# Performance work log

Measured on AMD Instinct MI355X. Metric: run time of the kernel, lower is better.

The kernel has to match this reference:

```python
import jax, jax.numpy as jnp
import numpy as np
import math

B, S, D, H, NH = 2, 2048, 1024, 16, 8
DK = D // H


def setup_inputs() -> dict:
    key = jax.random.key(0)
    ks = jax.random.split(key, 10)
    s = 1.0 / math.sqrt(D)
    return {
        "x": jax.random.normal(ks[0], (B, S, D), jnp.float32),
        "Wq": jax.random.normal(ks[1], (D, D), jnp.float32) * s,
        "bq": jnp.zeros((D,), jnp.float32),
        "Wk": jax.random.normal(ks[2], (D, D), jnp.float32) * s,
        "bk": jnp.zeros((D,), jnp.float32),
        "Wv": jax.random.normal(ks[3], (D, D), jnp.float32) * s,
        "bv": jnp.zeros((D,), jnp.float32),
        "Wo": jax.random.normal(ks[4], (D, D), jnp.float32) * s,
        "bo": jnp.zeros((D,), jnp.float32),
        "R": jax.random.normal(ks[5], (NH, DK), jnp.float32),
    }


def reference(x, Wq, bq, Wk, bk, Wv, bv, Wo, bo, R):
    b, s, _ = x.shape
    # projections -> [B, S, H, DK]
    Q = (x @ Wq + bq).reshape(b, s, H, DK)
    K = (x @ Wk + bk).reshape(b, s, H, DK)
    V = (x @ Wv + bv).reshape(b, s, H, DK)
    # LSH buckets: argmax over random projections -> [B, S, H] -> [B, H, S]
    qb = jnp.argmax(jnp.einsum('bshd,nd->bshn', Q, R), axis=-1).transpose(0, 2, 1)
    kb = jnp.argmax(jnp.einsum('bshd,nd->bshn', K, R), axis=-1).transpose(0, 2, 1)
    # bucket-equality mask [B, H, S, S]
    mask = qb[:, :, :, None] == kb[:, :, None, :]
    # attention: [B, H, S, S]
    scores = jnp.einsum('bihd,bjhd->bhij', Q, K) / jnp.sqrt(jnp.float32(DK))
    scores = jnp.where(mask, scores, -jnp.inf)
    probs = jax.nn.softmax(scores, axis=-1)
    out = jnp.einsum('bhij,bjhd->bihd', probs, V).reshape(b, s, D)
    return out @ Wo + bo
```

## Files before the change

kernel.cpp:

```cpp
#include <hip/hip_runtime.h>
#include <hip/hip_bf16.h>


typedef __bf16 bf16;
typedef __bf16 bf16x8 __attribute__((ext_vector_type(8)));
typedef __bf16 bf16x4 __attribute__((ext_vector_type(4)));
typedef float f32x4 __attribute__((ext_vector_type(4)));

#define DEV static __device__ __forceinline__

DEV f32x4 zero4() { f32x4 z; z[0]=0.f; z[1]=0.f; z[2]=0.f; z[3]=0.f; return z; }

DEV f32x4 mfma_bf16(bf16x8 a, bf16x8 b, f32x4 c) {
  return __builtin_amdgcn_mfma_f32_16x16x32_bf16(a, b, c, 0, 0, 0);
}

DEV void load_lds16(const bf16* g, bf16* l) {
  __builtin_amdgcn_global_load_lds(
      (const __attribute__((address_space(1))) void*)g,
      (__attribute__((address_space(3))) void*)l, 16, 0, 0);
}

#define B_  2
#define S_  2048
#define D_  1024
#define H_  16
#define NH_ 8
#define DK_ 64
#define M_  4096
#define QPAD 2560
#define NQT  40

__global__ void k_cast_split(const float* __restrict__ x, bf16* __restrict__ xh,
                             bf16* __restrict__ xm, bf16* __restrict__ xl) {
  int i = (blockIdx.x * 256 + threadIdx.x) * 4;
  f32x4 v = *(const f32x4*)(x + i);
  bf16x4 oh, om, ol;
#pragma unroll
  for (int j = 0; j < 4; j++) {
    float f = v[j];
    bf16 h = (bf16)f;
    float rm = f - (float)h;
    bf16 m = (bf16)rm;
    float rl = rm - (float)m;
    oh[j] = h; om[j] = m; ol[j] = (bf16)rl;
  }
  *(bf16x4*)(xh + i) = oh;
  *(bf16x4*)(xm + i) = om;
  *(bf16x4*)(xl + i) = ol;
}

__global__ void k_transW(const float* __restrict__ W0, const float* __restrict__ W1,
                         const float* __restrict__ W2, const float* __restrict__ W3,
                         bf16* __restrict__ T0, bf16* __restrict__ T1,
                         bf16* __restrict__ T2, bf16* __restrict__ T3) {
  __shared__ float tile[64][65];
  const float* W = blockIdx.z == 0 ? W0 : blockIdx.z == 1 ? W1 : blockIdx.z == 2 ? W2 : W3;
  bf16* Wt = blockIdx.z == 0 ? T0 : blockIdx.z == 1 ? T1 : blockIdx.z == 2 ? T2 : T3;
  int k0 = blockIdx.x * 64, n0 = blockIdx.y * 64;
  int c = threadIdx.x & 63, r4 = threadIdx.x >> 6;
#pragma unroll
  for (int i = 0; i < 16; i++) {
    int r = r4 * 16 + i;
    tile[r][c] = W[(k0 + r) * D_ + n0 + c];
  }
  __syncthreads();
#pragma unroll
  for (int i = 0; i < 16; i++) {
    int r = r4 * 16 + i;
    Wt[(n0 + r) * D_ + k0 + c] = (bf16)tile[c][r];
  }
}

__global__ void k_computeP(const float* __restrict__ Wq, const float* __restrict__ Wk,
                           const float* __restrict__ R, float* __restrict__ P) {
  int d = blockIdx.x;
  int t = threadIdx.x;
  int hn = t & 127, h = hn >> 3, n = hn & 7;
  const float* W = (t < 128) ? Wq : Wk;
  const float* wrow = W + d * D_ + h * 64;
  const float* rrow = R + n * 64;
  float acc = 0.f;
#pragma unroll 8
  for (int k = 0; k < 64; k++) acc += wrow[k] * rrow[k];
  P[d * 256 + t] = acc;
}

__global__ void k_transP(const float* __restrict__ P, bf16* __restrict__ Pth,
                         bf16* __restrict__ Ptm, bf16* __restrict__ Ptl) {
  __shared__ float tile[64][65];
  int k0 = blockIdx.x * 64, n0 = blockIdx.y * 64;
  int c = threadIdx.x & 63, r4 = threadIdx.x >> 6;
#pragma unroll
  for (int i = 0; i < 16; i++) {
    int r = r4 * 16 + i;
    tile[r][c] = P[(k0 + r) * 256 + n0 + c];
  }
  __syncthreads();
#pragma unroll
  for (int i = 0; i < 16; i++) {
    int r = r4 * 16 + i;
    float v = tile[c][r];
    bf16 h = (bf16)v;
    float rm = v - (float)h;
    bf16 m = (bf16)rm;
    bf16 l = (bf16)(rm - (float)m);
    int o = (n0 + r) * D_ + k0 + c;
    Pth[o] = h; Ptm[o] = m; Ptl[o] = l;
  }
}

__global__ void k_bterm(const float* __restrict__ bq, const float* __restrict__ bk,
                        const float* __restrict__ R, float* __restrict__ bt) {
  int t = threadIdx.x;
  const float* b = (t < 128) ? bq : bk;
  int hn = t & 127, h = hn >> 3, n = hn & 7;
  float acc = 0.f;
#pragma unroll 8
  for (int k = 0; k < 64; k++) acc += b[h * 64 + k] * R[n * 64 + k];
  bt[t] = acc;
}

__global__ __launch_bounds__(256) void k_lgemm(const bf16* __restrict__ xh,
                                               const bf16* __restrict__ xm,
                                               const bf16* __restrict__ xl,
                                               const bf16* __restrict__ Pth,
                                               const bf16* __restrict__ Ptm,
                                               const bf16* __restrict__ Ptl,
                                               const float* __restrict__ bt,
                                               int* __restrict__ qb,
                                               int* __restrict__ kb) {
  __shared__ bf16 Ls[6][64 * 32];
  const int t = threadIdx.x;
  const int m0 = blockIdx.x * 64, n0 = blockIdx.y * 64;
  const int lane = t & 63, w = t >> 6;
  const int lm = lane & 15, qd = lane >> 4;
  const bf16* src6[6] = {xh, xm, xl, Pth, Ptm, Ptl};
  const int srow = lane >> 2, sseg = lane & 3;

  f32x4 acc[4];
#pragma unroll
  for (int nb = 0; nb < 4; nb++) acc[nb] = zero4();

  for (int k0 = 0; k0 < D_; k0 += 32) {
    __syncthreads();
#pragma unroll
    for (int r3 = 0; r3 < 6; r3++) {
      int ii = r3 * 4 + w;
      int tt = ii >> 2, qq = ii & 3;
      int base = (tt < 3 ? m0 : n0) + qq * 16 + srow;
      load_lds16(&src6[tt][base * D_ + k0 + sseg * 8], &Ls[tt][qq * 16 * 32]);
    }
    __syncthreads();
    bf16x8 af[3], bfr[3][4];
#pragma unroll
    for (int i3 = 0; i3 < 3; i3++) {
      af[i3] = *(const bf16x8*)&Ls[i3][(w * 16 + lm) * 32 + qd * 8];
#pragma unroll
      for (int nb = 0; nb < 4; nb++)
        bfr[i3][nb] = *(const bf16x8*)&Ls[3 + i3][(nb * 16 + lm) * 32 + qd * 8];
    }
#pragma unroll
    for (int nb = 0; nb < 4; nb++) {
      f32x4 a = acc[nb];
      a = mfma_bf16(af[0], bfr[0][nb], a);
      a = mfma_bf16(af[0], bfr[1][nb], a);
      a = mfma_bf16(af[1], bfr[0][nb], a);
      a = mfma_bf16(af[0], bfr[2][nb], a);
      a = mfma_bf16(af[2], bfr[0][nb], a);
      a = mfma_bf16(af[1], bfr[1][nb], a);
      acc[nb] = a;
    }
  }

#pragma unroll
  for (int nb = 0; nb < 4; nb++) {
    int n = n0 + nb * 16 + lm;
    float btv = bt[n];
#pragma unroll
    for (int r = 0; r < 4; r++) {
      float v = acc[nb][r] + btv;
      int idx = lm & 7;
#pragma unroll
      for (int mask = 1; mask <= 4; mask <<= 1) {
        float pv = __shfl_xor(v, mask);
        int pi = __shfl_xor(idx, mask);
        if (pv > v || (pv == v && pi < idx)) { v = pv; idx = pi; }
      }
      if ((lm & 7) == 0) {
        int m = m0 + w * 16 + qd * 4 + r;
        int g = n >> 3;
        int sel = g >> 4, head = g & 15;
        int bb = m >> 11, s = m & 2047;
        (sel ? kb : qb)[(bb * H_ + head) * S_ + s] = idx;
      }
    }
  }
}

__global__ __launch_bounds__(256) void k_sort(const int* __restrict__ qb,
                                              const int* __restrict__ kb,
                                              int* __restrict__ qidx,
                                              int* __restrict__ kidx,
                                              int2* __restrict__ meta) {
  __shared__ int cnt[8][257];
  __shared__ int bst[2][9];
  __shared__ int tot[2][8];
  const int bh = blockIdx.x;
  const int t = threadIdx.x;
  for (int which = 0; which < 2; which++) {
    const int* src = (which ? kb : qb) + bh * S_;
    int* dst = (which ? kidx : qidx) + bh * QPAD;
    for (int i = t; i < QPAD; i += 256) dst[i] = -1;
    int vals[8];
    int lc[8] = {0, 0, 0, 0, 0, 0, 0, 0};
#pragma unroll
    for (int j = 0; j < 8; j++) { int b = src[t * 8 + j]; vals[j] = b; lc[b]++; }
#pragma unroll
    for (int b = 0; b < 8; b++) cnt[b][t] = lc[b];
    __syncthreads();
    if (t < 8) {
      int run = 0;
      for (int i = 0; i < 256; i++) { int c = cnt[t][i]; cnt[t][i] = run; run += c; }
      tot[which][t] = run;
    }
    __syncthreads();
    if (t == 0) {
      int pos = 0;
      for (int b = 0; b < 8; b++) {
        bst[which][b] = pos;
        pos += (tot[which][b] + 63) & ~63;
      }
      bst[which][8] = pos;
    }
    __syncthreads();
    int run2[8] = {0, 0, 0, 0, 0, 0, 0, 0};
#pragma unroll
    for (int j = 0; j < 8; j++) {
      int b = vals[j];
      int pos = bst[which][b] + cnt[b][t] + run2[b]++;
      dst[pos] = t * 8 + j;
    }
    __syncthreads();
  }
  if (t == 0) {
    for (int tt = 0; tt < NQT; tt++) meta[bh * NQT + tt] = make_int2(0, 0);
    for (int b = 0; b < 8; b++) {
      int t0 = bst[0][b] >> 6;
      int nt = ((tot[0][b] + 63) & ~63) >> 6;
      int ks = bst[1][b];
      int nkt = (tot[1][b] + 63) >> 6;
      for (int tt = t0; tt < t0 + nt; tt++)
        meta[bh * NQT + tt] = make_int2(ks, nkt);
    }
  }
}

template <int MODE>
__global__ __launch_bounds__(256) void k_gemm128(
    const bf16* __restrict__ A,
    const bf16* __restrict__ Bt0, const bf16* __restrict__ Bt1,
    const bf16* __restrict__ Bt2,
    const float* __restrict__ bi0, const float* __restrict__ bi1,
    const float* __restrict__ bi2,
    void* __restrict__ o0, void* __restrict__ o1, void* __restrict__ o2) {
  __shared__ bf16 Al[128 * 32];
  __shared__ bf16 Bl[128 * 32];
  const int t = threadIdx.x;
  const int lane = t & 63, w = t >> 6;
  const int m0 = blockIdx.x * 128;
  const int mat = blockIdx.y >> 3;
  const int n0 = (blockIdx.y & 7) * 128;
  const bf16* Bt = mat == 0 ? Bt0 : (mat == 1 ? Bt1 : Bt2);
  const float* bias = mat == 0 ? bi0 : (mat == 1 ? bi1 : bi2);
  void* out = mat == 0 ? o0 : (mat == 1 ? o1 : o2);
  const int lm = lane & 15, qd = lane >> 4;
  const int wm = w >> 1, wn = w & 1;
  const int srow = lane >> 2, sseg = lane & 3;

  f32x4 acc[4][4];
#pragma unroll
  for (int i = 0; i < 4; i++)
#pragma unroll
    for (int j = 0; j < 4; j++) acc[i][j] = zero4();

  for (int k0 = 0; k0 < D_; k0 += 32) {
    __syncthreads();
    load_lds16(&A[(m0 + w * 16 + srow) * D_ + k0 + sseg * 8],
               &Al[(w * 16) * 32]);
    load_lds16(&A[(m0 + 64 + w * 16 + srow) * D_ + k0 + sseg * 8],
               &Al[(64 + w * 16) * 32]);
    load_lds16(&Bt[(n0 + w * 16 + srow) * D_ + k0 + sseg * 8],
               &Bl[(w * 16) * 32]);
    load_lds16(&Bt[(n0 + 64 + w * 16 + srow) * D_ + k0 + sseg * 8],
               &Bl[(64 + w * 16) * 32]);
    __syncthreads();
    bf16x8 af[4], bfr[4];
#pragma unroll
    for (int i = 0; i < 4; i++)
      af[i] = *(const bf16x8*)&Al[(wm * 64 + i * 16 + lm) * 32 + qd * 8];
#pragma unroll
    for (int j = 0; j < 4; j++)
      bfr[j] = *(const bf16x8*)&Bl[(wn * 64 + j * 16 + lm) * 32 + qd * 8];
#pragma unroll
    for (int i = 0; i < 4; i++)
#pragma unroll
      for (int j = 0; j < 4; j++) acc[i][j] = mfma_bf16(af[i], bfr[j], acc[i][j]);
  }

#pragma unroll
  for (int j = 0; j < 4; j++) {
    int n = n0 + wn * 64 + j * 16 + lm;
    float bv = bias[n];
#pragma unroll
    for (int i = 0; i < 4; i++) {
      int mbase = m0 + wm * 64 + i * 16 + qd * 4;
#pragma unroll
      for (int r = 0; r < 4; r++) {
        int m = mbase + r;
        float v = acc[i][j][r] + bv;
        if (MODE == 0) {
          int bb = m >> 11, s = m & 2047, hh = n >> 6, d = n & 63;
          ((bf16*)out)[((bb * H_ + hh) * S_ + s) * DK_ + d] = (bf16)v;
        } else {
          ((float*)out)[m * D_ + n] = v;
        }
      }
    }
  }
}

__global__ __launch_bounds__(256) void k_attn(const bf16* __restrict__ Q,
                                              const bf16* __restrict__ K,
                                              const bf16* __restrict__ V,
                                              const int* __restrict__ qidx,
                                              const int* __restrict__ kidx,
                                              const int2* __restrict__ meta,
                                              bf16* __restrict__ O) {
  constexpr int LDK = 72;
  __shared__ bf16 Kl[64 * LDK];
  __shared__ bf16 Vl[64 * LDK];
  __shared__ bf16 Pl[64 * LDK];
  __shared__ int kbl[64];
  __shared__ int qsl[64];
  const int t = threadIdx.x;
  const int qt = blockIdx.x, h = blockIdx.y, b = blockIdx.z;
  const int lane = t & 63, w = t >> 6;
  const int lm = lane & 15, qd = lane >> 4;
  const int bh = b * H_ + h;

  const int2 mt = meta[bh * NQT + qt];
  const int kstart = mt.x, nkt = mt.y;

  if (t < 64) qsl[t] = qidx[bh * QPAD + qt * 64 + t];
  __syncthreads();

  if (nkt == 0) {
#pragma unroll
    for (int r = 0; r < 4; r++) {
      int qs = qsl[w * 16 + qd * 4 + r];
      if (qs >= 0)
#pragma unroll
        for (int nb = 0; nb < 4; nb++)
          O[((b * S_ + qs) * H_ + h) * DK_ + nb * 16 + lm] = (bf16)0.f;
    }
    return;
  }

  int qrow = qsl[w * 16 + lm];
  const bf16* Qp = Q + (bh * S_ + (qrow < 0 ? 0 : qrow)) * DK_;
  bf16x8 qf0 = *(const bf16x8*)(Qp + qd * 8);
  bf16x8 qf1 = *(const bf16x8*)(Qp + 32 + qd * 8);

  f32x4 oacc[4];
  float mrun[4], lrun[4];
#pragma unroll
  for (int nb = 0; nb < 4; nb++) oacc[nb] = zero4();
#pragma unroll
  for (int r = 0; r < 4; r++) { mrun[r] = -1e30f; lrun[r] = 0.f; }

  const bf16* Kbase = K + bh * S_ * DK_;
  const bf16* Vbase = V + bh * S_ * DK_;
  const int* kix = kidx + bh * QPAD + kstart;

  for (int kt = 0; kt < nkt; kt++) {
    const int kt0 = kt * 64;
    __syncthreads();
    if (t < 64) kbl[t] = kix[kt0 + t];
#pragma unroll
    for (int ss = 0; ss < 2; ss++) {
      int seg = t + ss * 256;
      int row = seg >> 3, sg = seg & 7;
      int ki = kix[kt0 + row]; ki = ki < 0 ? 0 : ki;
      *(bf16x8*)&Kl[row * LDK + sg * 8] =
          *(const bf16x8*)&Kbase[ki * DK_ + sg * 8];
    }
#pragma unroll
    for (int ss = 0; ss < 2; ss++) {
      int seg = t + ss * 256;
      int vrow = seg & 63, vsg = seg >> 6;
      int ki = kix[kt0 + vrow]; ki = ki < 0 ? 0 : ki;
      bf16x8 v8 = *(const bf16x8*)&Vbase[ki * DK_ + vsg * 8];
#pragma unroll
      for (int j = 0; j < 8; j++) Vl[(vsg * 8 + j) * LDK + vrow] = v8[j];
    }
    __syncthreads();

    f32x4 sc[4];
#pragma unroll
    for (int nb = 0; nb < 4; nb++) {
      bf16x8 kf0 = *(const bf16x8*)&Kl[(nb * 16 + lm) * LDK + qd * 8];
      bf16x8 kf1 = *(const bf16x8*)&Kl[(nb * 16 + lm) * LDK + 32 + qd * 8];
      f32x4 z = zero4();
      z = mfma_bf16(qf0, kf0, z);
      z = mfma_bf16(qf1, kf1, z);
      sc[nb] = z;
    }
#pragma unroll
    for (int nb = 0; nb < 4; nb++) {
      bool valid = kbl[nb * 16 + lm] >= 0;
#pragma unroll
      for (int r = 0; r < 4; r++)
        sc[nb][r] = valid ? sc[nb][r] * 0.125f : -1e30f;
    }
    float mnew[4], alpha[4], rs[4];
#pragma unroll
    for (int r = 0; r < 4; r++) {
      float tm = fmaxf(fmaxf(sc[0][r], sc[1][r]), fmaxf(sc[2][r], sc[3][r]));
      tm = fmaxf(tm, __shfl_xor(tm, 1));
      tm = fmaxf(tm, __shfl_xor(tm, 2));
      tm = fmaxf(tm, __shfl_xor(tm, 4));
      tm = fmaxf(tm, __shfl_xor(tm, 8));
      mnew[r] = fmaxf(mrun[r], tm);
      alpha[r] = __expf(mrun[r] - mnew[r]);
      mrun[r] = mnew[r];
      rs[r] = 0.f;
    }
#pragma unroll
    for (int nb = 0; nb < 4; nb++)
#pragma unroll
      for (int r = 0; r < 4; r++) {
        float p = (sc[nb][r] > -1e29f) ? __expf(sc[nb][r] - mnew[r]) : 0.f;
        sc[nb][r] = p;
        rs[r] += p;
      }
#pragma unroll
    for (int r = 0; r < 4; r++) {
      float s = rs[r];
      s += __shfl_xor(s, 1);
      s += __shfl_xor(s, 2);
      s += __shfl_xor(s, 4);
      s += __shfl_xor(s, 8);
      lrun[r] = lrun[r] * alpha[r] + s;
    }
#pragma unroll
    for (int nb = 0; nb < 4; nb++)
#pragma unroll
      for (int r = 0; r < 4; r++) oacc[nb][r] *= alpha[r];
#pragma unroll
    for (int nb = 0; nb < 4; nb++)
#pragma unroll
      for (int r = 0; r < 4; r++)
        Pl[(w * 16 + qd * 4 + r) * LDK + nb * 16 + lm] = (bf16)sc[nb][r];
    __syncthreads();
    bf16x8 pa0 = *(const bf16x8*)&Pl[(w * 16 + lm) * LDK + qd * 8];
    bf16x8 pa1 = *(const bf16x8*)&Pl[(w * 16 + lm) * LDK + 32 + qd * 8];
#pragma unroll
    for (int nb = 0; nb < 4; nb++) {
      bf16x8 vf0 = *(const bf16x8*)&Vl[(nb * 16 + lm) * LDK + qd * 8];
      bf16x8 vf1 = *(const bf16x8*)&Vl[(nb * 16 + lm) * LDK + 32 + qd * 8];
      oacc[nb] = mfma_bf16(pa0, vf0, oacc[nb]);
      oacc[nb] = mfma_bf16(pa1, vf1, oacc[nb]);
    }
  }
#pragma unroll
  for (int r = 0; r < 4; r++) {
    int qs = qsl[w * 16 + qd * 4 + r];
    if (qs < 0) continue;
    float l = lrun[r];
    float inv = (l > 0.f) ? 1.f / l : 0.f;
#pragma unroll
    for (int nb = 0; nb < 4; nb++)
      O[((b * S_ + qs) * H_ + h) * DK_ + nb * 16 + lm] = (bf16)(oacc[nb][r] * inv);
  }
}

extern "C" void kernel_launch(void* const* d_in, const int* in_sizes, int n_in,
                              void* d_out, int out_size, void* d_ws, size_t ws_size,
                              hipStream_t stream) {
  (void)in_sizes; (void)n_in; (void)out_size; (void)ws_size;
  const float* x  = (const float*)d_in[0];
  const float* Wq = (const float*)d_in[1];
  const float* bq = (const float*)d_in[2];
  const float* Wk = (const float*)d_in[3];
  const float* bk = (const float*)d_in[4];
  const float* Wv = (const float*)d_in[5];
  const float* bv = (const float*)d_in[6];
  const float* Wo = (const float*)d_in[7];
  const float* bo = (const float*)d_in[8];
  const float* R  = (const float*)d_in[9];

  char* ws = (char*)d_ws;
  bf16*  xh   = (bf16*)(ws + 0);
  bf16*  Qb   = (bf16*)(ws + 8388608);
  bf16*  Kb   = (bf16*)(ws + 16777216);
  bf16*  Vb   = (bf16*)(ws + 25165824);
  bf16*  Ob   = (bf16*)(ws + 33554432);
  bf16*  xm   = (bf16*)(ws + 33554432);
  bf16*  Wtq  = (bf16*)(ws + 41943040);
  bf16*  Wtk  = (bf16*)(ws + 44040192);
  bf16*  Wtv  = (bf16*)(ws + 46137344);
  bf16*  Wto  = (bf16*)(ws + 48234496);
  float* Pfull= (float*)(ws + 50331648);
  int*   qbuf = (int*)(ws + 51380224);
  int*   kbuf = (int*)(ws + 51642368);
  float* bt   = (float*)(ws + 51904512);
  bf16*  Pth  = (bf16*)(ws + 51905536);
  bf16*  Ptm  = (bf16*)(ws + 52429824);
  bf16*  Ptl  = (bf16*)(ws + 52954112);
  int*   qidxp= (int*)(ws + 53478400);
  int*   kidxp= (int*)(ws + 53806080);
  int2*  meta = (int2*)(ws + 54133760);
  bf16*  xl   = (bf16*)d_out;

  k_cast_split<<<dim3(4096), dim3(256), 0, stream>>>(x, xh, xm, xl);
  k_transW<<<dim3(16, 16, 4), dim3(256), 0, stream>>>(Wq, Wk, Wv, Wo,
                                                      Wtq, Wtk, Wtv, Wto);
  k_computeP<<<dim3(1024), dim3(256), 0, stream>>>(Wq, Wk, R, Pfull);
  k_bterm<<<dim3(1), dim3(256), 0, stream>>>(bq, bk, R, bt);
  k_transP<<<dim3(16, 4), dim3(256), 0, stream>>>(Pfull, Pth, Ptm, Ptl);

  k_lgemm<<<dim3(64, 4), dim3(256), 0, stream>>>(xh, xm, xl, Pth, Ptm, Ptl,
                                                 bt, qbuf, kbuf);
  k_sort<<<dim3(32), dim3(256), 0, stream>>>(qbuf, kbuf, qidxp, kidxp, meta);

  k_gemm128<0><<<dim3(32, 24), dim3(256), 0, stream>>>(
      xh, Wtq, Wtk, Wtv, bq, bk, bv, (void*)Qb, (void*)Kb, (void*)Vb);

  k_attn<<<dim3(NQT, H_, B_), dim3(256), 0, stream>>>(Qb, Kb, Vb, qidxp, kidxp,
                                                      meta, Ob);

  k_gemm128<2><<<dim3(32, 8), dim3(256), 0, stream>>>(
      Ob, Wto, Wto, Wto, bo, bo, bo, d_out, d_out, d_out);
}
```

Before: 251.5 us.

## Fuse prep kernels, merge LSH and QKV GEMMs, parallelize sort scan, smaller out-proj tiles

Combines the weight transpose, x cast, the projection matrix P and the bias term into a single prep launch. P is now computed directly in transposed, split form, so the fp32 intermediate and its transpose pass are gone. The LSH bucket GEMM now splits x into hi/mid/lo inside the kernel and shares one grid with the QKV projection GEMM, which removes the xm/xl buffers and a launch. The sort's serial per-bucket prefix scan becomes a wave-level shuffle scan, and the output projection uses 64x128 tiles to get more blocks. Risks are load imbalance between the two block types in the merged kernel and the LDS footprint of the larger shared arrays.

```diff
diff --git a/kernel.cpp b/kernel.cpp
--- a/kernel.cpp
+++ b/kernel.cpp
@@ -19,6 +19,13 @@
   __builtin_amdgcn_global_load_lds(
       (const __attribute__((address_space(1))) void*)g,
       (__attribute__((address_space(3))) void*)l, 16, 0, 0);
+}
+
+DEV void split3(float f, bf16& h, bf16& m, bf16& l) {
+  h = (bf16)f;
+  float rm = f - (float)h;
+  m = (bf16)rm;
+  l = (bf16)(rm - (float)m);
 }
 
 #define B_  2
@@ -31,168 +38,234 @@
 #define QPAD 2560
 #define NQT  40
 
-__global__ void k_cast_split(const float* __restrict__ x, bf16* __restrict__ xh,
-                             bf16* __restrict__ xm, bf16* __restrict__ xl) {
-  int i = (blockIdx.x * 256 + threadIdx.x) * 4;
-  f32x4 v = *(const f32x4*)(x + i);
-  bf16x4 oh, om, ol;
-#pragma unroll
-  for (int j = 0; j < 4; j++) {
-    float f = v[j];
-    bf16 h = (bf16)f;
-    float rm = f - (float)h;
-    bf16 m = (bf16)rm;
-    float rl = rm - (float)m;
-    oh[j] = h; om[j] = m; ol[j] = (bf16)rl;
-  }
-  *(bf16x4*)(xh + i) = oh;
-  *(bf16x4*)(xm + i) = om;
-  *(bf16x4*)(xl + i) = ol;
-}
-
-__global__ void k_transW(const float* __restrict__ W0, const float* __restrict__ W1,
-                         const float* __restrict__ W2, const float* __restrict__ W3,
-                         bf16* __restrict__ T0, bf16* __restrict__ T1,
-                         bf16* __restrict__ T2, bf16* __restrict__ T3) {
+__global__ __launch_bounds__(256) void k_prep(
+    const float* __restrict__ Wq, const float* __restrict__ Wk,
+    const float* __restrict__ Wv, const float* __restrict__ Wo,
+    const float* __restrict__ x, const float* __restrict__ bq,
+    const float* __restrict__ bk, const float* __restrict__ R,
+    bf16* __restrict__ Wtq, bf16* __restrict__ Wtk,
+    bf16* __restrict__ Wtv, bf16* __restrict__ Wto,
+    bf16* __restrict__ xh, bf16* __restrict__ Pth, bf16* __restrict__ Ptm,
+    bf16* __restrict__ Ptl, float* __restrict__ bt) {
   __shared__ float tile[64][65];
-  const float* W = blockIdx.z == 0 ? W0 : blockIdx.z == 1 ? W1 : blockIdx.z == 2 ? W2 : W3;
-  bf16* Wt = blockIdx.z == 0 ? T0 : blockIdx.z == 1 ? T1 : blockIdx.z == 2 ? T2 : T3;
-  int k0 = blockIdx.x * 64, n0 = blockIdx.y * 64;
-  int c = threadIdx.x & 63, r4 = threadIdx.x >> 6;
-#pragma unroll
-  for (int i = 0; i < 16; i++) {
-    int r = r4 * 16 + i;
-    tile[r][c] = W[(k0 + r) * D_ + n0 + c];
-  }
-  __syncthreads();
-#pragma unroll
-  for (int i = 0; i < 16; i++) {
-    int r = r4 * 16 + i;
-    Wt[(n0 + r) * D_ + k0 + c] = (bf16)tile[c][r];
-  }
-}
-
-__global__ void k_computeP(const float* __restrict__ Wq, const float* __restrict__ Wk,
-                           const float* __restrict__ R, float* __restrict__ P) {
-  int d = blockIdx.x;
-  int t = threadIdx.x;
-  int hn = t & 127, h = hn >> 3, n = hn & 7;
-  const float* W = (t < 128) ? Wq : Wk;
-  const float* wrow = W + d * D_ + h * 64;
-  const float* rrow = R + n * 64;
-  float acc = 0.f;
+  __shared__ float Rl[512];
+  const int t = threadIdx.x;
+  const int z = blockIdx.z;
+  if (z < 4) {
+    const float* W = z == 0 ? Wq : z == 1 ? Wk : z == 2 ? Wv : Wo;
+    bf16* Wt = z == 0 ? Wtq : z == 1 ? Wtk : z == 2 ? Wtv : Wto;
+    int k0 = blockIdx.x * 64, n0 = blockIdx.y * 64;
+    int c = t & 63, r4 = t >> 6;
+#pragma unroll
+    for (int i = 0; i < 16; i++) {
+      int r = r4 * 16 + i;
+      tile[r][c] = W[(k0 + r) * D_ + n0 + c];
+    }
+    __syncthreads();
+#pragma unroll
+    for (int i = 0; i < 16; i++) {
+      int r = r4 * 16 + i;
+      Wt[(n0 + r) * D_ + k0 + c] = (bf16)tile[c][r];
+    }
+  } else if (z == 4) {
+    int bid = blockIdx.y * 16 + blockIdx.x;
+    int base = bid * 16384 + t * 4;
+#pragma unroll 4
+    for (int it = 0; it < 16; it++) {
+      int i = base + it * 1024;
+      f32x4 v = *(const f32x4*)(x + i);
+      bf16x4 o;
+#pragma unroll
+      for (int j = 0; j < 4; j++) o[j] = (bf16)v[j];
+      *(bf16x4*)(xh + i) = o;
+    }
+  } else {
+    int bid = blockIdx.y * 16 + blockIdx.x;
+    if (bid >= 64) return;
+    Rl[t] = R[t];
+    Rl[t + 256] = R[t + 256];
+    __syncthreads();
+    const int d0 = bid * 16;
+    const int sel = t >> 7, hn = t & 127, h = hn >> 3, n = hn & 7;
+    const float* W = sel ? Wk : Wq;
+    const float* Rr = &Rl[n * 64];
+    bf16x8 vh[2], vm[2], vl[2];
+#pragma unroll
+    for (int dl = 0; dl < 16; dl++) {
+      const float* wr = W + (d0 + dl) * D_ + h * 64;
+      float acc = 0.f;
+#pragma unroll
+      for (int k = 0; k < 64; k += 4) {
+        f32x4 wv = *(const f32x4*)(wr + k);
+        acc += (wv[0] * Rr[k] + wv[1] * Rr[k + 1]) +
+               (wv[2] * Rr[k + 2] + wv[3] * Rr[k + 3]);
+      }
+      bf16 hh, mm, ll;
+      split3(acc, hh, mm, ll);
+      vh[dl >> 3][dl & 7] = hh;
+      vm[dl >> 3][dl & 7] = mm;
+      vl[dl >> 3][dl & 7] = ll;
+    }
+    *(bf16x8*)&Pth[t * D_ + d0] = vh[0];
+    *(bf16x8*)&Pth[t * D_ + d0 + 8] = vh[1];
+    *(bf16x8*)&Ptm[t * D_ + d0] = vm[0];
+    *(bf16x8*)&Ptm[t * D_ + d0 + 8] = vm[1];
+    *(bf16x8*)&Ptl[t * D_ + d0] = vl[0];
+    *(bf16x8*)&Ptl[t * D_ + d0 + 8] = vl[1];
+    if (bid == 0) {
+      const float* bb = sel ? bk : bq;
+      float acc = 0.f;
 #pragma unroll 8
-  for (int k = 0; k < 64; k++) acc += wrow[k] * rrow[k];
-  P[d * 256 + t] = acc;
-}
-
-__global__ void k_transP(const float* __restrict__ P, bf16* __restrict__ Pth,
-                         bf16* __restrict__ Ptm, bf16* __restrict__ Ptl) {
-  __shared__ float tile[64][65];
-  int k0 = blockIdx.x * 64, n0 = blockIdx.y * 64;
-  int c = threadIdx.x & 63, r4 = threadIdx.x >> 6;
-#pragma unroll
-  for (int i = 0; i < 16; i++) {
-    int r = r4 * 16 + i;
-    tile[r][c] = P[(k0 + r) * 256 + n0 + c];
-  }
-  __syncthreads();
-#pragma unroll
-  for (int i = 0; i < 16; i++) {
-    int r = r4 * 16 + i;
-    float v = tile[c][r];
-    bf16 h = (bf16)v;
-    float rm = v - (float)h;
-    bf16 m = (bf16)rm;
-    bf16 l = (bf16)(rm - (float)m);
-    int o = (n0 + r) * D_ + k0 + c;
-    Pth[o] = h; Ptm[o] = m; Ptl[o] = l;
-  }
-}
-
-__global__ void k_bterm(const float* __restrict__ bq, const float* __restrict__ bk,
-                        const float* __restrict__ R, float* __restrict__ bt) {
-  int t = threadIdx.x;
-  const float* b = (t < 128) ? bq : bk;
-  int hn = t & 127, h = hn >> 3, n = hn & 7;
-  float acc = 0.f;
-#pragma unroll 8
-  for (int k = 0; k < 64; k++) acc += b[h * 64 + k] * R[n * 64 + k];
-  bt[t] = acc;
-}
-
-__global__ __launch_bounds__(256) void k_lgemm(const bf16* __restrict__ xh,
-                                               const bf16* __restrict__ xm,
-                                               const bf16* __restrict__ xl,
-                                               const bf16* __restrict__ Pth,
-                                               const bf16* __restrict__ Ptm,
-                                               const bf16* __restrict__ Ptl,
-                                               const float* __restrict__ bt,
-                                               int* __restrict__ qb,
-                                               int* __restrict__ kb) {
-  __shared__ bf16 Ls[6][64 * 32];
+      for (int k = 0; k < 64; k++) acc += bb[h * 64 + k] * Rr[k];
+      bt[t] = acc;
+    }
+  }
+}
+
+__global__ __launch_bounds__(256) void k_main(
+    const float* __restrict__ x, const bf16* __restrict__ xh,
+    const bf16* __restrict__ Wtq, const bf16* __restrict__ Wtk,
+    const bf16* __restrict__ Wtv, const float* __restrict__ bq,
+    const float* __restrict__ bk, const float* __restrict__ bv,
+    const bf16* __restrict__ Pth, const bf16* __restrict__ Ptm,
+    const bf16* __restrict__ Ptl, const float* __restrict__ bt,
+    bf16* __restrict__ Qb, bf16* __restrict__ Kb, bf16* __restrict__ Vb,
+    int* __restrict__ qb, int* __restrict__ kb) {
+  __shared__ __align__(16) bf16 SA[3][2048];
+  __shared__ __align__(16) bf16 SB[3][2048];
   const int t = threadIdx.x;
-  const int m0 = blockIdx.x * 64, n0 = blockIdx.y * 64;
   const int lane = t & 63, w = t >> 6;
   const int lm = lane & 15, qd = lane >> 4;
-  const bf16* src6[6] = {xh, xm, xl, Pth, Ptm, Ptl};
   const int srow = lane >> 2, sseg = lane & 3;
 
-  f32x4 acc[4];
-#pragma unroll
-  for (int nb = 0; nb < 4; nb++) acc[nb] = zero4();
-
-  for (int k0 = 0; k0 < D_; k0 += 32) {
-    __syncthreads();
-#pragma unroll
-    for (int r3 = 0; r3 < 6; r3++) {
-      int ii = r3 * 4 + w;
-      int tt = ii >> 2, qq = ii & 3;
-      int base = (tt < 3 ? m0 : n0) + qq * 16 + srow;
-      load_lds16(&src6[tt][base * D_ + k0 + sseg * 8], &Ls[tt][qq * 16 * 32]);
-    }
-    __syncthreads();
-    bf16x8 af[3], bfr[3][4];
-#pragma unroll
-    for (int i3 = 0; i3 < 3; i3++) {
-      af[i3] = *(const bf16x8*)&Ls[i3][(w * 16 + lm) * 32 + qd * 8];
-#pragma unroll
-      for (int nb = 0; nb < 4; nb++)
-        bfr[i3][nb] = *(const bf16x8*)&Ls[3 + i3][(nb * 16 + lm) * 32 + qd * 8];
+  if (blockIdx.y < 24) {
+    if (blockIdx.x >= 32) return;
+    bf16* Al = &SA[0][0];
+    bf16* Bl = &SB[0][0];
+    const int m0 = blockIdx.x * 128;
+    const int mat = blockIdx.y >> 3;
+    const int n0 = (blockIdx.y & 7) * 128;
+    const bf16* Bt = mat == 0 ? Wtq : (mat == 1 ? Wtk : Wtv);
+    const float* bias = mat == 0 ? bq : (mat == 1 ? bk : bv);
+    bf16* out = mat == 0 ? Qb : (mat == 1 ? Kb : Vb);
+    const int wm = w >> 1, wn = w & 1;
+
+    f32x4 acc[4][4];
+#pragma unroll
+    for (int i = 0; i < 4; i++)
+#pragma unroll
+      for (int j = 0; j < 4; j++) acc[i][j] = zero4();
+
+    for (int k0 = 0; k0 < D_; k0 += 32) {
+      __syncthreads();
+      load_lds16(&xh[(m0 + w * 16 + srow) * D_ + k0 + sseg * 8],
+                 &Al[(w * 16) * 32]);
+      load_lds16(&xh[(m0 + 64 + w * 16 + srow) * D_ + k0 + sseg * 8],
+                 &Al[(64 + w * 16) * 32]);
+      load_lds16(&Bt[(n0 + w * 16 + srow) * D_ + k0 + sseg * 8],
+                 &Bl[(w * 16) * 32]);
+      load_lds16(&Bt[(n0 + 64 + w * 16 + srow) * D_ + k0 + sseg * 8],
+                 &Bl[(64 + w * 16) * 32]);
+      __syncthreads();
+      bf16x8 af[4], bfr[4];
+#pragma unroll
+      for (int i = 0; i < 4; i++)
+        af[i] = *(const bf16x8*)&Al[(wm * 64 + i * 16 + lm) * 32 + qd * 8];
+#pragma unroll
+      for (int j = 0; j < 4; j++)
+        bfr[j] = *(const bf16x8*)&Bl[(wn * 64 + j * 16 + lm) * 32 + qd * 8];
+#pragma unroll
+      for (int i = 0; i < 4; i++)
+#pragma unroll
+        for (int j = 0; j < 4; j++)
+          acc[i][j] = mfma_bf16(af[i], bfr[j], acc[i][j]);
+    }
+#pragma unroll
+    for (int j = 0; j < 4; j++) {
+      int n = n0 + wn * 64 + j * 16 + lm;
+      float bv2 = bias[n];
+#pragma unroll
+      for (int i = 0; i < 4; i++) {
+        int mbase = m0 + wm * 64 + i * 16 + qd * 4;
+#pragma unroll
+        for (int r = 0; r < 4; r++) {
+          int m = mbase + r;
+          int bb = m >> 11, s = m & 2047, hh = n >> 6, d = n & 63;
+          out[((bb * H_ + hh) * S_ + s) * DK_ + d] = (bf16)(acc[i][j][r] + bv2);
+        }
+      }
+    }
+  } else {
+    const int m0 = blockIdx.x * 64, n0 = (blockIdx.y - 24) * 64;
+    f32x4 acc[4];
+#pragma unroll
+    for (int nb = 0; nb < 4; nb++) acc[nb] = zero4();
+    const int xrow = t >> 2, xc8 = (t & 3) * 8;
+
+    for (int k0 = 0; k0 < D_; k0 += 32) {
+      __syncthreads();
+      f32x4 xa = *(const f32x4*)&x[(m0 + xrow) * D_ + k0 + xc8];
+      f32x4 xb2 = *(const f32x4*)&x[(m0 + xrow) * D_ + k0 + xc8 + 4];
+      bf16x8 vh, vm, vl;
+#pragma unroll
+      for (int j = 0; j < 4; j++) {
+        bf16 hh, mm, ll;
+        split3(xa[j], hh, mm, ll);
+        vh[j] = hh; vm[j] = mm; vl[j] = ll;
+        split3(xb2[j], hh, mm, ll);
+        vh[4 + j] = hh; vm[4 + j] = mm; vl[4 + j] = ll;
+      }
+      *(bf16x8*)&SA[0][xrow * 32 + xc8] = vh;
+      *(bf16x8*)&SA[1][xrow * 32 + xc8] = vm;
+      *(bf16x8*)&SA[2][xrow * 32 + xc8] = vl;
+      load_lds16(&Pth[(n0 + w * 16 + srow) * D_ + k0 + sseg * 8],
+                 &SB[0][(w * 16) * 32]);
+      load_lds16(&Ptm[(n0 + w * 16 + srow) * D_ + k0 + sseg * 8],
+                 &SB[1][(w * 16) * 32]);
+      load_lds16(&Ptl[(n0 + w * 16 + srow) * D_ + k0 + sseg * 8],
+                 &SB[2][(w * 16) * 32]);
+      __syncthreads();
+      bf16x8 af[3], bfr[3][4];
+#pragma unroll
+      for (int i3 = 0; i3 < 3; i3++) {
+        af[i3] = *(const bf16x8*)&SA[i3][(w * 16 + lm) * 32 + qd * 8];
+#pragma unroll
+        for (int nb = 0; nb < 4; nb++)
+          bfr[i3][nb] = *(const bf16x8*)&SB[i3][(nb * 16 + lm) * 32 + qd * 8];
+      }
+#pragma unroll
+      for (int nb = 0; nb < 4; nb++) {
+        f32x4 a = acc[nb];
+        a = mfma_bf16(af[0], bfr[0][nb], a);
+        a = mfma_bf16(af[0], bfr[1][nb], a);
+        a = mfma_bf16(af[1], bfr[0][nb], a);
+        a = mfma_bf16(af[0], bfr[2][nb], a);
+        a = mfma_bf16(af[2], bfr[0][nb], a);
+        a = mfma_bf16(af[1], bfr[1][nb], a);
+        acc[nb] = a;
+      }
     }
 #pragma unroll
     for (int nb = 0; nb < 4; nb++) {
-      f32x4 a = acc[nb];
-      a = mfma_bf16(af[0], bfr[0][nb], a);
-      a = mfma_bf16(af[0], bfr[1][nb], a);
-      a = mfma_bf16(af[1], bfr[0][nb], a);
-      a = mfma_bf16(af[0], bfr[2][nb], a);
-      a = mfma_bf16(af[2], bfr[0][nb], a);
-      a = mfma_bf16(af[1], bfr[1][nb], a);
-      acc[nb] = a;
-    }
-  }
-
-#pragma unroll
-  for (int nb = 0; nb < 4; nb++) {
-    int n = n0 + nb * 16 + lm;
-    float btv = bt[n];
-#pragma unroll
-    for (int r = 0; r < 4; r++) {
-      float v = acc[nb][r] + btv;
-      int idx = lm & 7;
-#pragma unroll
-      for (int mask = 1; mask <= 4; mask <<= 1) {
-        float pv = __shfl_xor(v, mask);
-        int pi = __shfl_xor(idx, mask);
-        if (pv > v || (pv == v && pi < idx)) { v = pv; idx = pi; }
-      }
-      if ((lm & 7) == 0) {
-        int m = m0 + w * 16 + qd * 4 + r;
-        int g = n >> 3;
-        int sel = g >> 4, head = g & 15;
-        int bb = m >> 11, s = m & 2047;
-        (sel ? kb : qb)[(bb * H_ + head) * S_ + s] = idx;
+      int n = n0 + nb * 16 + lm;
+      float btv = bt[n];
+#pragma unroll
+      for (int r = 0; r < 4; r++) {
+        float v = acc[nb][r] + btv;
+        int idx = lm & 7;
+#pragma unroll
+        for (int mask = 1; mask <= 4; mask <<= 1) {
+          float pv = __shfl_xor(v, mask);
+          int pi = __shfl_xor(idx, mask);
+          if (pv > v || (pv == v && pi < idx)) { v = pv; idx = pi; }
+        }
+        if ((lm & 7) == 0) {
+          int m = m0 + w * 16 + qd * 4 + r;
+          int g = n >> 3;
+          int sel = g >> 4, head = g & 15;
+          int bb = m >> 11, s = m & 2047;
+          (sel ? kb : qb)[(bb * H_ + head) * S_ + s] = idx;
+        }
       }
     }
   }
@@ -208,6 +281,7 @@
   __shared__ int tot[2][8];
   const int bh = blockIdx.x;
   const int t = threadIdx.x;
+  const int lane = t & 63, w = t >> 6;
   for (int which = 0; which < 2; which++) {
     const int* src = (which ? kb : qb) + bh * S_;
     int* dst = (which ? kidx : qidx) + bh * QPAD;
@@ -219,10 +293,20 @@
 #pragma unroll
     for (int b = 0; b < 8; b++) cnt[b][t] = lc[b];
     __syncthreads();
-    if (t < 8) {
-      int run = 0;
-      for (int i = 0; i < 256; i++) { int c = cnt[t][i]; cnt[t][i] = run; run += c; }
-      tot[which][t] = run;
+    for (int bb = w; bb < 8; bb += 4) {
+      int carry = 0;
+      for (int round = 0; round < 4; round++) {
+        int v = cnt[bb][round * 64 + lane];
+        int inc = v;
+#pragma unroll
+        for (int off = 1; off < 64; off <<= 1) {
+          int u = __shfl_up(inc, off);
+          if (lane >= off) inc += u;
+        }
+        cnt[bb][round * 64 + lane] = carry + inc - v;
+        carry += __shfl(inc, 63);
+      }
+      if (lane == 0) tot[which][bb] = carry;
     }
     __syncthreads();
     if (t == 0) {
@@ -252,80 +336,6 @@
       int nkt = (tot[1][b] + 63) >> 6;
       for (int tt = t0; tt < t0 + nt; tt++)
         meta[bh * NQT + tt] = make_int2(ks, nkt);
-    }
-  }
-}
-
-template <int MODE>
-__global__ __launch_bounds__(256) void k_gemm128(
-    const bf16* __restrict__ A,
-    const bf16* __restrict__ Bt0, const bf16* __restrict__ Bt1,
-    const bf16* __restrict__ Bt2,
-    const float* __restrict__ bi0, const float* __restrict__ bi1,
-    const float* __restrict__ bi2,
-    void* __restrict__ o0, void* __restrict__ o1, void* __restrict__ o2) {
-  __shared__ bf16 Al[128 * 32];
-  __shared__ bf16 Bl[128 * 32];
-  const int t = threadIdx.x;
-  const int lane = t & 63, w = t >> 6;
-  const int m0 = blockIdx.x * 128;
-  const int mat = blockIdx.y >> 3;
-  const int n0 = (blockIdx.y & 7) * 128;
-  const bf16* Bt = mat == 0 ? Bt0 : (mat == 1 ? Bt1 : Bt2);
-  const float* bias = mat == 0 ? bi0 : (mat == 1 ? bi1 : bi2);
-  void* out = mat == 0 ? o0 : (mat == 1 ? o1 : o2);
-  const int lm = lane & 15, qd = lane >> 4;
-  const int wm = w >> 1, wn = w & 1;
-  const int srow = lane >> 2, sseg = lane & 3;
-
-  f32x4 acc[4][4];
-#pragma unroll
-  for (int i = 0; i < 4; i++)
-#pragma unroll
-    for (int j = 0; j < 4; j++) acc[i][j] = zero4();
-
-  for (int k0 = 0; k0 < D_; k0 += 32) {
-    __syncthreads();
-    load_lds16(&A[(m0 + w * 16 + srow) * D_ + k0 + sseg * 8],
-               &Al[(w * 16) * 32]);
-    load_lds16(&A[(m0 + 64 + w * 16 + srow) * D_ + k0 + sseg * 8],
-               &Al[(64 + w * 16) * 32]);
-    load_lds16(&Bt[(n0 + w * 16 + srow) * D_ + k0 + sseg * 8],
-               &Bl[(w * 16) * 32]);
-    load_lds16(&Bt[(n0 + 64 + w * 16 + srow) * D_ + k0 + sseg * 8],
-               &Bl[(64 + w * 16) * 32]);
-    __syncthreads();
-    bf16x8 af[4], bfr[4];
-#pragma unroll
-    for (int i = 0; i < 4; i++)
-      af[i] = *(const bf16x8*)&Al[(wm * 64 + i * 16 + lm) * 32 + qd * 8];
-#pragma unroll
-    for (int j = 0; j < 4; j++)
-      bfr[j] = *(const bf16x8*)&Bl[(wn * 64 + j * 16 + lm) * 32 + qd * 8];
-#pragma unroll
-    for (int i = 0; i < 4; i++)
-#pragma unroll
-      for (int j = 0; j < 4; j++) acc[i][j] = mfma_bf16(af[i], bfr[j], acc[i][j]);
-  }
-
-#pragma unroll
-  for (int j = 0; j < 4; j++) {
-    int n = n0 + wn * 64 + j * 16 + lm;
-    float bv = bias[n];
-#pragma unroll
-    for (int i = 0; i < 4; i++) {
-      int mbase = m0 + wm * 64 + i * 16 + qd * 4;
-#pragma unroll
-      for (int r = 0; r < 4; r++) {
-        int m = mbase + r;
-        float v = acc[i][j][r] + bv;
-        if (MODE == 0) {
-          int bb = m >> 11, s = m & 2047, hh = n >> 6, d = n & 63;
-          ((bf16*)out)[((bb * H_ + hh) * S_ + s) * DK_ + d] = (bf16)v;
-        } else {
-          ((float*)out)[m * D_ + n] = v;
-        }
-      }
     }
   }
 }
@@ -485,6 +495,60 @@
   }
 }
 
+__global__ __launch_bounds__(256) void k_gout(const bf16* __restrict__ A,
+                                              const bf16* __restrict__ Bt,
+                                              const float* __restrict__ bias,
+                                              float* __restrict__ out) {
+  __shared__ __align__(16) bf16 Al[64 * 32];
+  __shared__ __align__(16) bf16 Bl[128 * 32];
+  const int t = threadIdx.x;
+  const int lane = t & 63, w = t >> 6;
+  const int lm = lane & 15, qd = lane >> 4;
+  const int srow = lane >> 2, sseg = lane & 3;
+  const int m0 = blockIdx.x * 64, n0 = blockIdx.y * 128;
+  const int wm = w >> 1, wn = w & 1;
+
+  f32x4 acc[2][4];
+#pragma unroll
+  for (int i = 0; i < 2; i++)
+#pragma unroll
+    for (int j = 0; j < 4; j++) acc[i][j] = zero4();
+
+  for (int k0 = 0; k0 < D_; k0 += 32) {
+    __syncthreads();
+    load_lds16(&A[(m0 + w * 16 + srow) * D_ + k0 + sseg * 8],
+               &Al[(w * 16) * 32]);
+    load_lds16(&Bt[(n0 + w * 16 + srow) * D_ + k0 + sseg * 8],
+               &Bl[(w * 16) * 32]);
+    load_lds16(&Bt[(n0 + 64 + w * 16 + srow) * D_ + k0 + sseg * 8],
+               &Bl[(64 + w * 16) * 32]);
+    __syncthreads();
+    bf16x8 af[2], bfr[4];
+#pragma unroll
+    for (int i = 0; i < 2; i++)
+      af[i] = *(const bf16x8*)&Al[(wm * 32 + i * 16 + lm) * 32 + qd * 8];
+#pragma unroll
+    for (int j = 0; j < 4; j++)
+      bfr[j] = *(const bf16x8*)&Bl[(wn * 64 + j * 16 + lm) * 32 + qd * 8];
+#pragma unroll
+    for (int i = 0; i < 2; i++)
+#pragma unroll
+      for (int j = 0; j < 4; j++) acc[i][j] = mfma_bf16(af[i], bfr[j], acc[i][j]);
+  }
+#pragma unroll
+  for (int j = 0; j < 4; j++) {
+    int n = n0 + wn * 64 + j * 16 + lm;
+    float bv = bias[n];
+#pragma unroll
+    for (int i = 0; i < 2; i++) {
+      int mbase = m0 + wm * 32 + i * 16 + qd * 4;
+#pragma unroll
+      for (int r = 0; r < 4; r++)
+        out[(mbase + r) * D_ + n] = acc[i][j][r] + bv;
+    }
+  }
+}
+
 extern "C" void kernel_launch(void* const* d_in, const int* in_sizes, int n_in,
                               void* d_out, int out_size, void* d_ws, size_t ws_size,
                               hipStream_t stream) {
@@ -506,12 +570,10 @@
   bf16*  Kb   = (bf16*)(ws + 16777216);
   bf16*  Vb   = (bf16*)(ws + 25165824);
   bf16*  Ob   = (bf16*)(ws + 33554432);
-  bf16*  xm   = (bf16*)(ws + 33554432);
   bf16*  Wtq  = (bf16*)(ws + 41943040);
   bf16*  Wtk  = (bf16*)(ws + 44040192);
   bf16*  Wtv  = (bf16*)(ws + 46137344);
   bf16*  Wto  = (bf16*)(ws + 48234496);
-  float* Pfull= (float*)(ws + 50331648);
   int*   qbuf = (int*)(ws + 51380224);
   int*   kbuf = (int*)(ws + 51642368);
   float* bt   = (float*)(ws + 51904512);
@@ -521,25 +583,18 @@
   int*   qidxp= (int*)(ws + 53478400);
   int*   kidxp= (int*)(ws + 53806080);
   int2*  meta = (int2*)(ws + 54133760);
-  bf16*  xl   = (bf16*)d_out;
-
-  k_cast_split<<<dim3(4096), dim3(256), 0, stream>>>(x, xh, xm, xl);
-  k_transW<<<dim3(16, 16, 4), dim3(256), 0, stream>>>(Wq, Wk, Wv, Wo,
-                                                      Wtq, Wtk, Wtv, Wto);
-  k_computeP<<<dim3(1024), dim3(256), 0, stream>>>(Wq, Wk, R, Pfull);
-  k_bterm<<<dim3(1), dim3(256), 0, stream>>>(bq, bk, R, bt);
-  k_transP<<<dim3(16, 4), dim3(256), 0, stream>>>(Pfull, Pth, Ptm, Ptl);
-
-  k_lgemm<<<dim3(64, 4), dim3(256), 0, stream>>>(xh, xm, xl, Pth, Ptm, Ptl,
-                                                 bt, qbuf, kbuf);
+
+  k_prep<<<dim3(16, 16, 6), dim3(256), 0, stream>>>(
+      Wq, Wk, Wv, Wo, x, bq, bk, R, Wtq, Wtk, Wtv, Wto, xh, Pth, Ptm, Ptl, bt);
+
+  k_main<<<dim3(64, 28), dim3(256), 0, stream>>>(
+      x, xh, Wtq, Wtk, Wtv, bq, bk, bv, Pth, Ptm, Ptl, bt, Qb, Kb, Vb,
+      qbuf, kbuf);
+
   k_sort<<<dim3(32), dim3(256), 0, stream>>>(qbuf, kbuf, qidxp, kidxp, meta);
-
-  k_gemm128<0><<<dim3(32, 24), dim3(256), 0, stream>>>(
-      xh, Wtq, Wtk, Wtv, bq, bk, bv, (void*)Qb, (void*)Kb, (void*)Vb);
 
   k_attn<<<dim3(NQT, H_, B_), dim3(256), 0, stream>>>(Qb, Kb, Vb, qidxp, kidxp,
                                                       meta, Ob);
 
-  k_gemm128<2><<<dim3(32, 8), dim3(256), 0, stream>>>(
-      Ob, Wto, Wto, Wto, bo, bo, bo, d_out, d_out, d_out);
-}
+  k_gout<<<dim3(64, 8), dim3(256), 0, stream>>>(Ob, Wto, bo, (float*)d_out);
+}
```

After: 240.8 us. -4.3%, faster.
